# Kernel optimization log

Hardware: AMD Instinct MI355X
Metric: run time of the kernel (lower is better)

The kernel has to match this reference:

```python
import jax, jax.numpy as jnp
import numpy as np

N_NODES = 100000
N_EDGES = 1600000
IN_DIM, HID_DIM, OUT_DIM = 384, 64, 64
DROP_P = 0.5


def setup_inputs() -> dict:
    key = jax.random.key(0)
    ks = jax.random.split(key, 9)
    x = jax.random.normal(ks[0], (N_NODES, IN_DIM), dtype=jnp.float32)
    edge_index = jax.random.randint(ks[1], (2, N_EDGES), 0, N_NODES, dtype=jnp.int64)
    edge_weight = jax.random.uniform(ks[2], (N_EDGES,), dtype=jnp.float32)
    W1 = jax.random.normal(ks[3], (IN_DIM, HID_DIM), dtype=jnp.float32) * (1.0 / np.sqrt(IN_DIM))
    b1 = jnp.zeros((HID_DIM,), dtype=jnp.float32)
    W2 = jax.random.normal(ks[4], (HID_DIM, OUT_DIM), dtype=jnp.float32) * (1.0 / np.sqrt(HID_DIM))
    b2 = jnp.zeros((OUT_DIM,), dtype=jnp.float32)
    drop_mask1 = jax.random.bernoulli(ks[5], 1.0 - DROP_P, (N_NODES, IN_DIM))
    drop_mask2 = jax.random.bernoulli(ks[6], 1.0 - DROP_P, (N_NODES, HID_DIM))
    return {"x": x, "edge_index": edge_index, "edge_weight": edge_weight,
            "W1": W1, "b1": b1, "W2": W2, "b2": b2,
            "drop_mask1": drop_mask1, "drop_mask2": drop_mask2}


def _gcn_conv(h, W, b, src, dst, edge_weight, n_nodes):
    # GCNConv: linear transform first (smaller dim), then normalized sparse aggregation
    h = h @ W                                        # [N, d_out]
    msg = h[src] * edge_weight[:, None]              # gather over edges [E, d_out]
    agg = jax.ops.segment_sum(msg, dst, num_segments=n_nodes)  # scatter-add [N, d_out]
    return agg + b


def reference(x, edge_index, edge_weight, W1, b1, W2, b2, drop_mask1, drop_mask2):
    scale = 1.0 / (1.0 - DROP_P)
    src, dst = edge_index[0], edge_index[1]
    n = x.shape[0]
    h = x * drop_mask1.astype(x.dtype) * scale                  # dropout (training)
    h = jax.nn.relu(_gcn_conv(h, W1, b1, src, dst, edge_weight, n))
    h = h * drop_mask2.astype(h.dtype) * scale                  # dropout (training)
    return _gcn_conv(h, W2, b2, src, dst, edge_weight, n)
```

## Files before the change

### kernel.cpp

```cpp
#include <hip/hip_runtime.h>
#include <hip/hip_bf16.h>
#include <stdint.h>

#define N_NODES 100000
#define N_EDGES 1600000
#define IN_DIM  384
#define HID_DIM 64
#define NPART   8
#define NP      (NPART * N_NODES)
#define SCAN8_NB 782
#define SCANF_NB 391
#define EGRID   2048

typedef __attribute__((ext_vector_type(8))) short short8_t;
typedef __attribute__((ext_vector_type(4))) float f32x4;

__global__ void k_detect(const uint32_t* __restrict__ ei,
                         const uint32_t* __restrict__ m1,
                         int* __restrict__ flags) {
    int l = threadIdx.x;
    uint32_t hi = ei[2 * l + 1];
    int ei64 = __all(hi == 0u);

    uint32_t maxb = 0;
    int bf = 0, f16 = 0, hib = 0;
    for (int i = 0; i < 4; ++i) {
        uint32_t w = m1[l * 4 + i];
        uint32_t b0 = w & 0xffu, b1 = (w >> 8) & 0xffu,
                 b2 = (w >> 16) & 0xffu, b3 = (w >> 24) & 0xffu;
        uint32_t mb = b0 > b1 ? b0 : b1;
        uint32_t mb2 = b2 > b3 ? b2 : b3;
        mb = mb > mb2 ? mb : mb2;
        maxb = maxb > mb ? maxb : mb;
        if ((w & 0xffffu) == 0x3f80u) bf = 1;
        if ((w & 0xffffu) == 0x3c00u) f16 = 1;
        if ((b1 | b2 | b3) != 0u) hib = 1;
    }
    int small  = __all(maxb <= 1u);
    int anybf  = __any(bf);
    int anyf16 = __any(f16);
    int anyhib = __any(hib);
    if (l == 0) {
        flags[0] = ei64;
        int mm;
        if (small)                 mm = anyhib ? 3 : 4;
        else if (anybf || anyf16)  mm = 0;
        else                       mm = 2;
        flags[1] = mm;
    }
}

__device__ __forceinline__ float mask_at(const void* p, int mode, long idx) {
    if (mode == 0) return ((const uint16_t*)p)[idx] ? 2.0f : 0.0f;
    if (mode == 2) return ((const float*)p)[idx] != 0.0f ? 2.0f : 0.0f;
    if (mode == 3) return ((const uint8_t*)p)[idx] ? 2.0f : 0.0f;
    return ((const int*)p)[idx] ? 2.0f : 0.0f;
}

__device__ __forceinline__ void load_edge(const int* p32, int mode64, long e,
                                          int& s, int& d) {
    if (mode64) { s = p32[2 * e]; d = p32[2 * (N_EDGES + e)]; }
    else        { s = p32[e];     d = p32[N_EDGES + e]; }
}

__device__ __forceinline__ ushort f2bf(float f) {
    uint32_t u = __float_as_uint(f);
    return (ushort)((u + 0x7fffu + ((u >> 16) & 1u)) >> 16);
}
__device__ __forceinline__ float bf2f(ushort h) {
    return __uint_as_float(((uint32_t)h) << 16);
}

__global__ __launch_bounds__(256) void k_hist8(const void* __restrict__ ei,
                                               uint32_t* __restrict__ deg8,
                                               const int* __restrict__ flags) {
    const int mode64 = flags[0];
    const int* p32 = (const int*)ei;
    const long pbase = (long)(blockIdx.x & (NPART - 1)) * N_NODES;
    for (long e = (long)blockIdx.x * 256 + threadIdx.x; e < N_EDGES;
         e += (long)EGRID * 256) {
        int s, d; load_edge(p32, mode64, e, s, d);
        atomicAdd(&deg8[pbase + d], 1u);
    }
}

__global__ __launch_bounds__(256) void k_scanA8(const uint32_t* __restrict__ deg,
                                                uint32_t* __restrict__ partials) {
    __shared__ uint32_t sbuf[256];
    long base = (long)blockIdx.x * 1024 + threadIdx.x * 4;
    uint32_t s = 0;
    if (base + 3 < NP) {
        uint4 v = *(const uint4*)&deg[base];
        s = v.x + v.y + v.z + v.w;
    } else {
        for (int j = 0; j < 4; ++j) if (base + j < NP) s += deg[base + j];
    }
    sbuf[threadIdx.x] = s;
    __syncthreads();
    for (int off = 128; off > 0; off >>= 1) {
        if (threadIdx.x < off) sbuf[threadIdx.x] += sbuf[threadIdx.x + off];
        __syncthreads();
    }
    if (threadIdx.x == 0) partials[blockIdx.x] = sbuf[0];
}

__global__ __launch_bounds__(1024) void k_scanB8(const uint32_t* __restrict__ partials,
                                                 uint32_t* __restrict__ poff,
                                                 uint32_t* __restrict__ starts) {
    __shared__ uint32_t sbuf[1024];
    int t = threadIdx.x;
    uint32_t v = t < SCAN8_NB ? partials[t] : 0u;
    sbuf[t] = v;
    __syncthreads();
    for (int off = 1; off < 1024; off <<= 1) {
        uint32_t add = t >= off ? sbuf[t - off] : 0u;
        __syncthreads();
        sbuf[t] += add;
        __syncthreads();
    }
    if (t < SCAN8_NB) poff[t] = sbuf[t] - v;
    if (t == SCAN8_NB - 1) starts[NP] = sbuf[t];
}

__global__ __launch_bounds__(256) void k_scanC8(const uint32_t* __restrict__ deg,
                                                const uint32_t* __restrict__ poff,
                                                uint32_t* __restrict__ starts,
                                                uint32_t* __restrict__ cur) {
    __shared__ uint32_t sbuf[256];
    long base = (long)blockIdx.x * 1024 + threadIdx.x * 4;
    uint32_t v[4] = {0, 0, 0, 0};
    if (base + 3 < NP) {
        uint4 q = *(const uint4*)&deg[base];
        v[0] = q.x; v[1] = q.y; v[2] = q.z; v[3] = q.w;
    } else {
        for (int j = 0; j < 4; ++j) if (base + j < NP) v[j] = deg[base + j];
    }
    uint32_t ts = v[0] + v[1] + v[2] + v[3];
    sbuf[threadIdx.x] = ts;
    __syncthreads();
    for (int off = 1; off < 256; off <<= 1) {
        uint32_t add = threadIdx.x >= off ? sbuf[threadIdx.x - off] : 0u;
        __syncthreads();
        sbuf[threadIdx.x] += add;
        __syncthreads();
    }
    uint32_t run = poff[blockIdx.x] + sbuf[threadIdx.x] - ts;
    for (int j = 0; j < 4; ++j) {
        if (base + j < NP) {
            starts[base + j] = run;
            cur[base + j]    = run;
            run += v[j];
        }
    }
}

__global__ __launch_bounds__(256) void k_degsum(const uint32_t* __restrict__ deg8,
                                                uint32_t* __restrict__ degF) {
    int n = blockIdx.x * 256 + threadIdx.x;
    if (n < N_NODES) {
        uint32_t s = 0;
#pragma unroll
        for (int p = 0; p < NPART; ++p) s += deg8[(long)p * N_NODES + n];
        degF[n] = s;
    }
}

__global__ __launch_bounds__(256) void k_scanAF(const uint32_t* __restrict__ deg,
                                                uint32_t* __restrict__ partials) {
    __shared__ uint32_t sbuf[256];
    int idx = blockIdx.x * 256 + threadIdx.x;
    uint32_t v = idx < N_NODES ? deg[idx] : 0u;
    sbuf[threadIdx.x] = v;
    __syncthreads();
    for (int off = 128; off > 0; off >>= 1) {
        if (threadIdx.x < off) sbuf[threadIdx.x] += sbuf[threadIdx.x + off];
        __syncthreads();
    }
    if (threadIdx.x == 0) partials[blockIdx.x] = sbuf[0];
}

__global__ __launch_bounds__(512) void k_scanBF(const uint32_t* __restrict__ partials,
                                                uint32_t* __restrict__ poff,
                                                uint32_t* __restrict__ starts) {
    __shared__ uint32_t sbuf[512];
    int t = threadIdx.x;
    uint32_t v = t < SCANF_NB ? partials[t] : 0u;
    sbuf[t] = v;
    __syncthreads();
    for (int off = 1; off < 512; off <<= 1) {
        uint32_t add = t >= off ? sbuf[t - off] : 0u;
        __syncthreads();
        sbuf[t] += add;
        __syncthreads();
    }
    if (t < SCANF_NB) poff[t] = sbuf[t] - v;
    if (t == SCANF_NB - 1) starts[N_NODES] = sbuf[t];
}

__global__ __launch_bounds__(256) void k_scanCF(const uint32_t* __restrict__ deg,
                                                const uint32_t* __restrict__ poff,
                                                uint32_t* __restrict__ starts) {
    __shared__ uint32_t sbuf[256];
    int idx = blockIdx.x * 256 + threadIdx.x;
    uint32_t v = idx < N_NODES ? deg[idx] : 0u;
    sbuf[threadIdx.x] = v;
    __syncthreads();
    for (int off = 1; off < 256; off <<= 1) {
        uint32_t add = threadIdx.x >= off ? sbuf[threadIdx.x - off] : 0u;
        __syncthreads();
        sbuf[threadIdx.x] += add;
        __syncthreads();
    }
    if (idx < N_NODES) starts[idx] = poff[blockIdx.x] + sbuf[threadIdx.x] - v;
}

__global__ __launch_bounds__(256) void k_reorder8(const void* __restrict__ ei,
                                                  const float* __restrict__ ew,
                                                  uint32_t* __restrict__ cur8,
                                                  int2* __restrict__ sorted,
                                                  const int* __restrict__ flags) {
    const int mode64 = flags[0];
    const int* p32 = (const int*)ei;
    const long pbase = (long)(blockIdx.x & (NPART - 1)) * N_NODES;
    for (long e = (long)blockIdx.x * 256 + threadIdx.x; e < N_EDGES;
         e += (long)EGRID * 256) {
        int s, d; load_edge(p32, mode64, e, s, d);
        float w = ew[e];
        uint32_t pos = atomicAdd(&cur8[pbase + d], 1u);
        sorted[pos] = make_int2(s, __float_as_int(w));
    }
}

__global__ __launch_bounds__(256) void k_merge(const int2* __restrict__ tmp,
                                               const uint32_t* __restrict__ starts8,
                                               const uint32_t* __restrict__ startsF,
                                               int2* __restrict__ dst) {
    const int lane = threadIdx.x & 63;
    const int n = blockIdx.x * 4 + (threadIdx.x >> 6);
    uint32_t sv = 0, lv = 0;
    if (lane < NPART) {
        sv = starts8[(long)lane * N_NODES + n];
        lv = starts8[(long)lane * N_NODES + n + 1] - sv;
    }
    uint32_t pv = lv;
#pragma unroll
    for (int off = 1; off < 8; off <<= 1) {
        uint32_t t = __shfl_up(pv, off, 64);
        if (lane >= off) pv += t;
    }
    uint32_t ev_ = pv - lv;
    uint32_t tot = __shfl((int)pv, 7, 64);
    uint32_t base = startsF[n];
    uint32_t e1v = __shfl((int)ev_, 1, 64), e2v = __shfl((int)ev_, 2, 64),
             e3v = __shfl((int)ev_, 3, 64), e4v = __shfl((int)ev_, 4, 64),
             e5v = __shfl((int)ev_, 5, 64), e6v = __shfl((int)ev_, 6, 64),
             e7v = __shfl((int)ev_, 7, 64);
    uint32_t s0v = __shfl((int)sv, 0, 64), s1v = __shfl((int)sv, 1, 64),
             s2v = __shfl((int)sv, 2, 64), s3v = __shfl((int)sv, 3, 64),
             s4v = __shfl((int)sv, 4, 64), s5v = __shfl((int)sv, 5, 64),
             s6v = __shfl((int)sv, 6, 64), s7v = __shfl((int)sv, 7, 64);
    for (uint32_t i = lane; i < tot; i += 64) {
        uint32_t eb = 0, sb = s0v;
        if (i >= e1v) { eb = e1v; sb = s1v; }
        if (i >= e2v) { eb = e2v; sb = s2v; }
        if (i >= e3v) { eb = e3v; sb = s3v; }
        if (i >= e4v) { eb = e4v; sb = s4v; }
        if (i >= e5v) { eb = e5v; sb = s5v; }
        if (i >= e6v) { eb = e6v; sb = s6v; }
        if (i >= e7v) { eb = e7v; sb = s7v; }
        dst[base + i] = tmp[sb + (i - eb)];
    }
}

__global__ __launch_bounds__(256) void k_packW(const float* __restrict__ W1,
                                               ushort* __restrict__ Wpack) {
    const int ks = blockIdx.x;
    const int t  = threadIdx.x;
    const int nt = t >> 6, l = t & 63;
    ushort hs[8], ls[8];
#pragma unroll
    for (int j = 0; j < 8; ++j) {
        float wv = W1[(ks * 32 + (l >> 4) * 8 + j) * 64 + nt * 16 + (l & 15)];
        ushort h = f2bf(wv);
        hs[j] = h;
        ls[j] = f2bf(wv - bf2f(h));
    }
    *(short8_t*)&Wpack[((8 * ks + nt) * 64 + l) * 8]     = *(short8_t*)hs;
    *(short8_t*)&Wpack[((8 * ks + 4 + nt) * 64 + l) * 8] = *(short8_t*)ls;
}

__global__ __launch_bounds__(256) void k1_mfma(
        const float* __restrict__ x, const void* __restrict__ m1,
        const ushort* __restrict__ Wpack, ushort* __restrict__ Hb,
        const int* __restrict__ flags) {
    const int mmode = flags[1];
    const int t = threadIdx.x;
    const int l = t & 63, w = t >> 6;
    const int node0 = blockIdx.x * 64;
    const long row = node0 + w * 16 + (l & 15);
    const int kq = (l >> 4) * 8;
    const bool valid = row < N_NODES;

    f32x4 acc[4];
#pragma unroll
    for (int i = 0; i < 4; ++i) acc[i] = (f32x4)0.0f;

    for (int ks = 0; ks < 12; ++ks) {
        float xv[8];
        if (valid) {
            long gb = row * IN_DIM + ks * 32 + kq;
            float4 x0 = *(const float4*)(x + gb);
            float4 x1 = *(const float4*)(x + gb + 4);
            xv[0] = x0.x; xv[1] = x0.y; xv[2] = x0.z; xv[3] = x0.w;
            xv[4] = x1.x; xv[5] = x1.y; xv[6] = x1.z; xv[7] = x1.w;
            float mv[8];
            if (mmode == 0) {
                const ushort* mp = (const ushort*)m1 + gb;
                ushort4 a = *(const ushort4*)mp;
                ushort4 b = *(const ushort4*)(mp + 4);
                mv[0] = a.x ? 2.f : 0.f; mv[1] = a.y ? 2.f : 0.f;
                mv[2] = a.z ? 2.f : 0.f; mv[3] = a.w ? 2.f : 0.f;
                mv[4] = b.x ? 2.f : 0.f; mv[5] = b.y ? 2.f : 0.f;
                mv[6] = b.z ? 2.f : 0.f; mv[7] = b.w ? 2.f : 0.f;
            } else if (mmode == 2) {
                const float* mp = (const float*)m1 + gb;
                float4 a = *(const float4*)mp;
                float4 b = *(const float4*)(mp + 4);
                mv[0] = a.x != 0.f ? 2.f : 0.f; mv[1] = a.y != 0.f ? 2.f : 0.f;
                mv[2] = a.z != 0.f ? 2.f : 0.f; mv[3] = a.w != 0.f ? 2.f : 0.f;
                mv[4] = b.x != 0.f ? 2.f : 0.f; mv[5] = b.y != 0.f ? 2.f : 0.f;
                mv[6] = b.z != 0.f ? 2.f : 0.f; mv[7] = b.w != 0.f ? 2.f : 0.f;
            } else if (mmode == 3) {
                uint2 mb = *(const uint2*)((const uint8_t*)m1 + gb);
#pragma unroll
                for (int j = 0; j < 4; ++j) {
                    mv[j]     = ((mb.x >> (8 * j)) & 0xffu) ? 2.f : 0.f;
                    mv[4 + j] = ((mb.y >> (8 * j)) & 0xffu) ? 2.f : 0.f;
                }
            } else {
                const int* mp = (const int*)m1 + gb;
                int4 a = *(const int4*)mp;
                int4 b = *(const int4*)(mp + 4);
                mv[0] = a.x ? 2.f : 0.f; mv[1] = a.y ? 2.f : 0.f;
                mv[2] = a.z ? 2.f : 0.f; mv[3] = a.w ? 2.f : 0.f;
                mv[4] = b.x ? 2.f : 0.f; mv[5] = b.y ? 2.f : 0.f;
                mv[6] = b.z ? 2.f : 0.f; mv[7] = b.w ? 2.f : 0.f;
            }
#pragma unroll
            for (int j = 0; j < 8; ++j) xv[j] *= mv[j];
        } else {
#pragma unroll
            for (int j = 0; j < 8; ++j) xv[j] = 0.0f;
        }
        ushort ap[8];
#pragma unroll
        for (int j = 0; j < 8; ++j) ap[j] = f2bf(xv[j]);
        short8_t ah = *(short8_t*)ap;

#pragma unroll
        for (int nt = 0; nt < 4; ++nt) {
            short8_t bh = *(const short8_t*)&Wpack[((8 * ks + nt) * 64 + l) * 8];
            short8_t bl = *(const short8_t*)&Wpack[((8 * ks + 4 + nt) * 64 + l) * 8];
            acc[nt] = __builtin_amdgcn_mfma_f32_16x16x32_bf16(ah, bh, acc[nt], 0, 0, 0);
            acc[nt] = __builtin_amdgcn_mfma_f32_16x16x32_bf16(ah, bl, acc[nt], 0, 0, 0);
        }
    }
    const int r0 = (l >> 4) * 4;
#pragma unroll
    for (int nt = 0; nt < 4; ++nt) {
#pragma unroll
        for (int r = 0; r < 4; ++r) {
            long node = node0 + w * 16 + r0 + r;
            if (node < N_NODES)
                Hb[node * 64 + nt * 16 + (l & 15)] = f2bf(acc[nt][r]);
        }
    }
}

__device__ __forceinline__ float agg_nodeF(const ushort* __restrict__ Hb,
                                           const int2* __restrict__ sorted,
                                           const uint32_t* __restrict__ starts,
                                           int n, int lane) {
    uint32_t e = starts[n], e1 = starts[n + 1];
    float acc0 = 0.f, acc1 = 0.f, acc2 = 0.f, acc3 = 0.f;
    while (e < e1) {
        uint32_t rem = e1 - e;
        uint32_t cnt = rem < 64u ? rem : 64u;
        uint32_t idx = e + (uint32_t)lane;
        if (idx >= e1) idx = e1 - 1;
        int2 my = sorted[idx];
        uint32_t j = 0;
        for (; j + 4 <= cnt; j += 4) {
            int sA = __shfl(my.x, (int)j + 0, 64), wA = __shfl(my.y, (int)j + 0, 64);
            int sB = __shfl(my.x, (int)j + 1, 64), wB = __shfl(my.y, (int)j + 1, 64);
            int sC = __shfl(my.x, (int)j + 2, 64), wC = __shfl(my.y, (int)j + 2, 64);
            int sD = __shfl(my.x, (int)j + 3, 64), wD = __shfl(my.y, (int)j + 3, 64);
            float vA = bf2f(Hb[(long)sA * 64 + lane]);
            float vB = bf2f(Hb[(long)sB * 64 + lane]);
            float vC = bf2f(Hb[(long)sC * 64 + lane]);
            float vD = bf2f(Hb[(long)sD * 64 + lane]);
            acc0 = fmaf(vA, __int_as_float(wA), acc0);
            acc1 = fmaf(vB, __int_as_float(wB), acc1);
            acc2 = fmaf(vC, __int_as_float(wC), acc2);
            acc3 = fmaf(vD, __int_as_float(wD), acc3);
        }
        for (; j < cnt; ++j) {
            int sA = __shfl(my.x, (int)j, 64), wA = __shfl(my.y, (int)j, 64);
            acc0 = fmaf(bf2f(Hb[(long)sA * 64 + lane]), __int_as_float(wA), acc0);
        }
        e += cnt;
    }
    return (acc0 + acc1) + (acc2 + acc3);
}

__global__ __launch_bounds__(256) void k_aggmlp(
        const ushort* __restrict__ Hb, const int2* __restrict__ sorted,
        const uint32_t* __restrict__ starts, const float* __restrict__ b1,
        const void* __restrict__ m2, const float* __restrict__ W2,
        ushort* __restrict__ H2b, const int* __restrict__ flags) {
    __shared__ float w2s[64 * 64];
    __shared__ float vbuf[4][64];
    const int mmode = flags[1];
    for (int i = threadIdx.x; i < 4096; i += 256) w2s[i] = W2[i];
    __syncthreads();

    const int lane = threadIdx.x & 63;
    const int w = threadIdx.x >> 6;
    const int n = blockIdx.x * 4 + w;
    float acc = agg_nodeF(Hb, sorted, starts, n, lane);
    float u = acc + b1[lane];
    u = u > 0.0f ? u : 0.0f;
    u *= mask_at(m2, mmode, (long)n * 64 + lane);
    vbuf[w][lane] = u;
    float h2 = 0.0f;
#pragma unroll
    for (int j = 0; j < 64; j += 4) {
        float4 v4 = *(const float4*)&vbuf[w][j];
        h2 = fmaf(v4.x, w2s[(j + 0) * 64 + lane], h2);
        h2 = fmaf(v4.y, w2s[(j + 1) * 64 + lane], h2);
        h2 = fmaf(v4.z, w2s[(j + 2) * 64 + lane], h2);
        h2 = fmaf(v4.w, w2s[(j + 3) * 64 + lane], h2);
    }
    H2b[(long)n * 64 + lane] = f2bf(h2);
}

__global__ __launch_bounds__(256) void k_agg(const ushort* __restrict__ Hb,
                                             const int2* __restrict__ sorted,
                                             const uint32_t* __restrict__ starts,
                                             const float* __restrict__ bias,
                                             float* __restrict__ dest) {
    const int lane = threadIdx.x & 63;
    const int n = blockIdx.x * 4 + (threadIdx.x >> 6);
    if (n >= N_NODES) return;
    float acc = bias[lane] + agg_nodeF(Hb, sorted, starts, n, lane);
    dest[(long)n * 64 + lane] = acc;
}

__global__ __launch_bounds__(256) void k_scatter(
        const ushort* __restrict__ Hb, const void* __restrict__ ei,
        const float* __restrict__ ew, float* __restrict__ dest,
        const int* __restrict__ flags) {
    const int mode64 = flags[0];
    const int lane = threadIdx.x & 63;
    const long wid = (long)blockIdx.x * 4 + (threadIdx.x >> 6);
    const long nw = (long)gridDim.x * 4;
    const int* p32 = (const int*)ei;
    for (long e = wid; e < N_EDGES; e += nw) {
        int s, d; load_edge(p32, mode64, e, s, d);
        float w = ew[e];
        float v = bf2f(Hb[(long)s * 64 + lane]) * w;
        atomicAdd(&dest[(long)d * 64 + lane], v);
    }
}

__global__ __launch_bounds__(256) void k3_mlp(
        const float* __restrict__ agg, const float* __restrict__ b1,
        const void* __restrict__ m2, const float* __restrict__ W2,
        ushort* __restrict__ H2b, const int* __restrict__ flags) {
    __shared__ float w2s[64 * 64];
    __shared__ float vbuf[4][64];
    const int mmode = flags[1];
    for (int i = threadIdx.x; i < 4096; i += 256) w2s[i] = W2[i];
    __syncthreads();
    const int lane = threadIdx.x & 63;
    const int w = threadIdx.x >> 6;
    const float bc = b1[lane];
    const long wid = (long)blockIdx.x * 4 + w;
    const long nw = (long)gridDim.x * 4;
    for (long n = wid; n < N_NODES; n += nw) {
        float u = agg[n * 64 + lane] + bc;
        u = u > 0.0f ? u : 0.0f;
        u *= mask_at(m2, mmode, n * 64 + lane);
        vbuf[w][lane] = u;
        float acc = 0.0f;
#pragma unroll
        for (int j = 0; j < 64; j += 4) {
            float4 v4 = *(const float4*)&vbuf[w][j];
            acc = fmaf(v4.x, w2s[(j + 0) * 64 + lane], acc);
            acc = fmaf(v4.y, w2s[(j + 1) * 64 + lane], acc);
            acc = fmaf(v4.z, w2s[(j + 2) * 64 + lane], acc);
            acc = fmaf(v4.w, w2s[(j + 3) * 64 + lane], acc);
        }
        H2b[n * 64 + lane] = f2bf(acc);
    }
}

__global__ void k_init_out(float* __restrict__ out, const float* __restrict__ b2) {
    const long total = (long)N_NODES * 16;
    for (long j = (long)blockIdx.x * 256 + threadIdx.x; j < total;
         j += (long)gridDim.x * 256) {
        ((float4*)out)[j] = ((const float4*)b2)[j & 15];
    }
}

extern "C" void kernel_launch(void* const* d_in, const int* in_sizes, int n_in,
                              void* d_out, int out_size, void* d_ws, size_t ws_size,
                              hipStream_t stream) {
    const float* x  = (const float*)d_in[0];
    const void*  ei = d_in[1];
    const float* ew = (const float*)d_in[2];
    const float* W1 = (const float*)d_in[3];
    const float* b1 = (const float*)d_in[4];
    const float* W2 = (const float*)d_in[5];
    const float* b2 = (const float*)d_in[6];
    const void*  m1 = d_in[7];
    const void*  m2 = d_in[8];
    float* out = (float*)d_out;

    char* ws = (char*)d_ws;
    size_t off = 0;
    auto alloc = [&](size_t bytes) {
        char* p = ws + off;
        off += (bytes + 255) & ~(size_t)255;
        return p;
    };
    int*    flags = (int*)alloc(32);
    ushort* Hb    = (ushort*)alloc((size_t)N_NODES * 64 * 2);
    ushort* H2b   = (ushort*)alloc((size_t)N_NODES * 64 * 2);
    int2*   sorted8 = (int2*)alloc((size_t)N_EDGES * 8);
    int2*   sortedF = (int2*)alloc((size_t)N_EDGES * 8);
    float*  AGG   = (float*)sorted8;
    uint32_t* starts8 = (uint32_t*)alloc((size_t)(NP + 64) * 4);
    uint32_t* cur8    = (uint32_t*)alloc((size_t)NP * 4);
    uint32_t* deg8    = (uint32_t*)alloc((size_t)NP * 4);
    uint32_t* degF    = (uint32_t*)alloc((size_t)N_NODES * 4);
    uint32_t* startsF = (uint32_t*)alloc((size_t)(N_NODES + 64) * 4);
    uint32_t* part8   = (uint32_t*)alloc((size_t)SCAN8_NB * 4);
    uint32_t* poff8   = (uint32_t*)alloc((size_t)SCAN8_NB * 4);
    uint32_t* partF   = (uint32_t*)alloc((size_t)SCANF_NB * 4);
    uint32_t* poffF   = (uint32_t*)alloc((size_t)SCANF_NB * 4);
    ushort*   Wpack   = (ushort*)alloc((size_t)12 * 8 * 64 * 8 * 2);
    size_t need = off;

    hipLaunchKernelGGL(k_detect, dim3(1), dim3(64), 0, stream,
                       (const uint32_t*)ei, (const uint32_t*)m1, flags);
    hipLaunchKernelGGL(k_packW, dim3(12), dim3(256), 0, stream, W1, Wpack);

    if (ws_size >= need) {
        hipMemsetAsync(deg8, 0, (size_t)NP * 4, stream);
        hipLaunchKernelGGL(k_hist8, dim3(EGRID), dim3(256), 0, stream,
                           ei, deg8, flags);
        hipLaunchKernelGGL(k_scanA8, dim3(SCAN8_NB), dim3(256), 0, stream,
                           deg8, part8);
        hipLaunchKernelGGL(k_scanB8, dim3(1), dim3(1024), 0, stream,
                           part8, poff8, starts8);
        hipLaunchKernelGGL(k_scanC8, dim3(SCAN8_NB), dim3(256), 0, stream,
                           deg8, poff8, starts8, cur8);
        hipLaunchKernelGGL(k_reorder8, dim3(EGRID), dim3(256), 0, stream,
                           ei, ew, cur8, sorted8, flags);
        hipLaunchKernelGGL(k_degsum, dim3(SCANF_NB), dim3(256), 0, stream,
                           deg8, degF);
        hipLaunchKernelGGL(k_scanAF, dim3(SCANF_NB), dim3(256), 0, stream,
                           degF, partF);
        hipLaunchKernelGGL(k_scanBF, dim3(1), dim3(512), 0, stream,
                           partF, poffF, startsF);
        hipLaunchKernelGGL(k_scanCF, dim3(SCANF_NB), dim3(256), 0, stream,
                           degF, poffF, startsF);
        hipLaunchKernelGGL(k_merge, dim3(N_NODES / 4), dim3(256), 0, stream,
                           sorted8, starts8, startsF, sortedF);
        hipLaunchKernelGGL(k1_mfma, dim3((N_NODES + 63) / 64), dim3(256), 0, stream,
                           x, m1, Wpack, Hb, flags);
        hipLaunchKernelGGL(k_aggmlp, dim3(N_NODES / 4), dim3(256), 0, stream,
                           Hb, sortedF, startsF, b1, m2, W2, H2b, flags);
        hipLaunchKernelGGL(k_agg, dim3(N_NODES / 4), dim3(256), 0, stream,
                           H2b, sortedF, startsF, b2, out);
    } else {
        hipMemsetAsync(AGG, 0, (size_t)N_NODES * 64 * 4, stream);
        hipLaunchKernelGGL(k1_mfma, dim3((N_NODES + 63) / 64), dim3(256), 0, stream,
                           x, m1, Wpack, Hb, flags);
        hipLaunchKernelGGL(k_scatter, dim3(4096), dim3(256), 0, stream,
                           Hb, ei, ew, AGG, flags);
        hipLaunchKernelGGL(k3_mlp, dim3(1024), dim3(256), 0, stream,
                           AGG, b1, m2, W2, H2b, flags);
        hipLaunchKernelGGL(k_init_out, dim3(2048), dim3(256), 0, stream, out, b2);
        hipLaunchKernelGGL(k_scatter, dim3(4096), dim3(256), 0, stream,
                           H2b, ei, ew, out, flags);
    }
}
```

Baseline: 718.9 us.

## Stage x tiles through swizzled LDS via global_load_lds in layer-1 MFMA kernel

Each k-step of the first-layer GEMM now loads a 64x32 fp32 tile of x cooperatively into a swizzled shared-memory buffer. It uses the direct global-to-LDS load builtin when the compiler has it, and a plain copy otherwise. Each lane then reads its MFMA A-fragment from LDS instead of doing strided per-row global loads. The goal is more coalesced global reads of the dominant 150MB input. In exchange, every k-step now costs two block barriers, there is no double buffering, and out-of-range rows are clamped rather than zeroed, so they still feed the MFMA but their results are never stored.

```diff
diff --git a/kernel.cpp b/kernel.cpp
--- a/kernel.cpp
+++ b/kernel.cpp
@@ -14,6 +14,15 @@
 
 typedef __attribute__((ext_vector_type(8))) short short8_t;
 typedef __attribute__((ext_vector_type(4))) float f32x4;
+
+#if defined(__has_builtin)
+# if __has_builtin(__builtin_amdgcn_global_load_lds)
+#  define HAS_GLL 1
+# endif
+#endif
+#ifndef HAS_GLL
+# define HAS_GLL 0
+#endif
 
 __global__ void k_detect(const uint32_t* __restrict__ ei,
                          const uint32_t* __restrict__ m1,
@@ -293,68 +302,94 @@
         const float* __restrict__ x, const void* __restrict__ m1,
         const ushort* __restrict__ Wpack, ushort* __restrict__ Hb,
         const int* __restrict__ flags) {
+    __shared__ float xt[2048];
+    char* xtb = (char*)xt;
     const int mmode = flags[1];
     const int t = threadIdx.x;
     const int l = t & 63, w = t >> 6;
     const int node0 = blockIdx.x * 64;
-    const long row = node0 + w * 16 + (l & 15);
+
+    const int srow0 = t >> 3;
+    const int srow1 = srow0 + 32;
+    const int scol0 = ((t & 7) * 16) ^ ((srow0 & 7) << 4);
+    const int scol1 = ((t & 7) * 16) ^ ((srow1 & 7) << 4);
+    long g0 = node0 + srow0; if (g0 >= N_NODES) g0 = N_NODES - 1;
+    long g1 = node0 + srow1; if (g1 >= N_NODES) g1 = N_NODES - 1;
+    const char* src0 = (const char*)x + g0 * (IN_DIM * 4) + scol0;
+    const char* src1 = (const char*)x + g1 * (IN_DIM * 4) + scol1;
+
+    const int fr = w * 16 + (l & 15);
     const int kq = (l >> 4) * 8;
-    const bool valid = row < N_NODES;
+    const int swz = (fr & 7) << 4;
+    const int p1 = (fr * 128 + (l >> 4) * 32) ^ swz;
+    const int p2 = (fr * 128 + (l >> 4) * 32 + 16) ^ swz;
+    long mrow = node0 + fr; if (mrow >= N_NODES) mrow = N_NODES - 1;
 
     f32x4 acc[4];
 #pragma unroll
     for (int i = 0; i < 4; ++i) acc[i] = (f32x4)0.0f;
 
     for (int ks = 0; ks < 12; ++ks) {
-        float xv[8];
-        if (valid) {
-            long gb = row * IN_DIM + ks * 32 + kq;
-            float4 x0 = *(const float4*)(x + gb);
-            float4 x1 = *(const float4*)(x + gb + 4);
-            xv[0] = x0.x; xv[1] = x0.y; xv[2] = x0.z; xv[3] = x0.w;
-            xv[4] = x1.x; xv[5] = x1.y; xv[6] = x1.z; xv[7] = x1.w;
-            float mv[8];
+#if HAS_GLL
+        __builtin_amdgcn_global_load_lds(
+            (const __attribute__((address_space(1))) void*)(src0 + ks * 128),
+            (__attribute__((address_space(3))) void*)(xtb + w * 1024), 16, 0, 0);
+        __builtin_amdgcn_global_load_lds(
+            (const __attribute__((address_space(1))) void*)(src1 + ks * 128),
+            (__attribute__((address_space(3))) void*)(xtb + 4096 + w * 1024), 16, 0, 0);
+#else
+        *(float4*)(xtb + t * 16)        = *(const float4*)(src0 + ks * 128);
+        *(float4*)(xtb + 4096 + t * 16) = *(const float4*)(src1 + ks * 128);
+#endif
+        uint4 mA = make_uint4(0, 0, 0, 0), mB = make_uint4(0, 0, 0, 0);
+        {
+            const long mgb = mrow * IN_DIM + ks * 32 + kq;
             if (mmode == 0) {
-                const ushort* mp = (const ushort*)m1 + gb;
-                ushort4 a = *(const ushort4*)mp;
-                ushort4 b = *(const ushort4*)(mp + 4);
-                mv[0] = a.x ? 2.f : 0.f; mv[1] = a.y ? 2.f : 0.f;
-                mv[2] = a.z ? 2.f : 0.f; mv[3] = a.w ? 2.f : 0.f;
-                mv[4] = b.x ? 2.f : 0.f; mv[5] = b.y ? 2.f : 0.f;
-                mv[6] = b.z ? 2.f : 0.f; mv[7] = b.w ? 2.f : 0.f;
+                mA = *(const uint4*)((const ushort*)m1 + mgb);
             } else if (mmode == 2) {
-                const float* mp = (const float*)m1 + gb;
-                float4 a = *(const float4*)mp;
-                float4 b = *(const float4*)(mp + 4);
-                mv[0] = a.x != 0.f ? 2.f : 0.f; mv[1] = a.y != 0.f ? 2.f : 0.f;
-                mv[2] = a.z != 0.f ? 2.f : 0.f; mv[3] = a.w != 0.f ? 2.f : 0.f;
-                mv[4] = b.x != 0.f ? 2.f : 0.f; mv[5] = b.y != 0.f ? 2.f : 0.f;
-                mv[6] = b.z != 0.f ? 2.f : 0.f; mv[7] = b.w != 0.f ? 2.f : 0.f;
+                mA = *(const uint4*)((const float*)m1 + mgb);
+                mB = *(const uint4*)((const float*)m1 + mgb + 4);
             } else if (mmode == 3) {
-                uint2 mb = *(const uint2*)((const uint8_t*)m1 + gb);
-#pragma unroll
-                for (int j = 0; j < 4; ++j) {
-                    mv[j]     = ((mb.x >> (8 * j)) & 0xffu) ? 2.f : 0.f;
-                    mv[4 + j] = ((mb.y >> (8 * j)) & 0xffu) ? 2.f : 0.f;
-                }
+                uint2 v = *(const uint2*)((const uint8_t*)m1 + mgb);
+                mA.x = v.x; mA.y = v.y;
             } else {
-                const int* mp = (const int*)m1 + gb;
-                int4 a = *(const int4*)mp;
-                int4 b = *(const int4*)(mp + 4);
-                mv[0] = a.x ? 2.f : 0.f; mv[1] = a.y ? 2.f : 0.f;
-                mv[2] = a.z ? 2.f : 0.f; mv[3] = a.w ? 2.f : 0.f;
-                mv[4] = b.x ? 2.f : 0.f; mv[5] = b.y ? 2.f : 0.f;
-                mv[6] = b.z ? 2.f : 0.f; mv[7] = b.w ? 2.f : 0.f;
+                mA = *(const uint4*)((const int*)m1 + mgb);
+                mB = *(const uint4*)((const int*)m1 + mgb + 4);
             }
-#pragma unroll
-            for (int j = 0; j < 8; ++j) xv[j] *= mv[j];
+        }
+        __syncthreads();
+
+        float4 xv0 = *(const float4*)(xtb + p1);
+        float4 xv1 = *(const float4*)(xtb + p2);
+        float xv[8] = {xv0.x, xv0.y, xv0.z, xv0.w, xv1.x, xv1.y, xv1.z, xv1.w};
+
+        float mv[8];
+        if (mmode == 0) {
+            uint mw[4] = {mA.x, mA.y, mA.z, mA.w};
+#pragma unroll
+            for (int j = 0; j < 4; ++j) {
+                mv[2 * j]     = (mw[j] & 0xffffu)  ? 2.f : 0.f;
+                mv[2 * j + 1] = (mw[j] >> 16)      ? 2.f : 0.f;
+            }
+        } else if (mmode == 2) {
+            uint mw[8] = {mA.x, mA.y, mA.z, mA.w, mB.x, mB.y, mB.z, mB.w};
+#pragma unroll
+            for (int j = 0; j < 8; ++j)
+                mv[j] = __uint_as_float(mw[j]) != 0.f ? 2.f : 0.f;
+        } else if (mmode == 3) {
+            uint mw[2] = {mA.x, mA.y};
+#pragma unroll
+            for (int j = 0; j < 8; ++j)
+                mv[j] = ((mw[j >> 2] >> (8 * (j & 3))) & 0xffu) ? 2.f : 0.f;
         } else {
-#pragma unroll
-            for (int j = 0; j < 8; ++j) xv[j] = 0.0f;
-        }
+            uint mw[8] = {mA.x, mA.y, mA.z, mA.w, mB.x, mB.y, mB.z, mB.w};
+#pragma unroll
+            for (int j = 0; j < 8; ++j) mv[j] = mw[j] ? 2.f : 0.f;
+        }
+
         ushort ap[8];
 #pragma unroll
-        for (int j = 0; j < 8; ++j) ap[j] = f2bf(xv[j]);
+        for (int j = 0; j < 8; ++j) ap[j] = f2bf(xv[j] * mv[j]);
         short8_t ah = *(short8_t*)ap;
 
 #pragma unroll
@@ -364,6 +399,7 @@
             acc[nt] = __builtin_amdgcn_mfma_f32_16x16x32_bf16(ah, bh, acc[nt], 0, 0, 0);
             acc[nt] = __builtin_amdgcn_mfma_f32_16x16x32_bf16(ah, bl, acc[nt], 0, 0, 0);
         }
+        __syncthreads();
     }
     const int r0 = (l >> 4) * 4;
 #pragma unroll
```

Result: no change. 719.7 us (+0.1%).
